# Kernel optimization log

Measured on AMD Instinct MI355X. Metric: run time of the kernel, lower is better.

The kernel has to match this reference:

```python
import jax, jax.numpy as jnp
import numpy as np

V, D, H, L, B, T = 32000, 1024, 1024, 4, 32, 128
PAD_ID = 0


def setup_inputs() -> dict:
    key = jax.random.key(0)
    ks = jax.random.split(key, 12)
    s = lambda fan: 1.0 / np.sqrt(fan)
    dec_input = jax.random.randint(ks[0], (B, T), 0, V)
    h0 = jax.random.normal(ks[1], (L, B, H), jnp.float32)
    c0 = jax.random.normal(ks[2], (L, B, H), jnp.float32)
    emb = jax.random.normal(ks[3], (V, D), jnp.float32) * 0.02
    emb = emb.at[PAD_ID].set(0.0)
    # all layers have input size H (layer0 input = embedding_dim = H)
    W_ih = jax.random.uniform(ks[4], (L, 4 * H, H), jnp.float32, -s(H), s(H))
    W_hh = jax.random.uniform(ks[5], (L, 4 * H, H), jnp.float32, -s(H), s(H))
    b_ih = jax.random.uniform(ks[6], (L, 4 * H), jnp.float32, -s(H), s(H))
    b_hh = jax.random.uniform(ks[7], (L, 4 * H), jnp.float32, -s(H), s(H))
    cls_W = jax.random.uniform(ks[8], (V, H), jnp.float32, -s(H), s(H))
    cls_b = jax.random.uniform(ks[9], (V,), jnp.float32, -s(H), s(H))
    return {"dec_input": dec_input, "h0": h0, "c0": c0, "emb": emb,
            "W_ih": W_ih, "W_hh": W_hh, "b_ih": b_ih, "b_hh": b_hh,
            "cls_W": cls_W, "cls_b": cls_b}


def _lstm_stack_step(carry, x_t, W_ih, W_hh, b_ih, b_hh):
    # carry: (h [L,B,H], c [L,B,H]); x_t: [B,H]
    h, c = carry
    inp = x_t
    hs, cs = [], []
    n_layers = W_ih.shape[0]
    for l in range(n_layers):
        gates = inp @ W_ih[l].T + h[l] @ W_hh[l].T + b_ih[l] + b_hh[l]
        i_g, f_g, g_g, o_g = jnp.split(gates, 4, axis=-1)
        c_new = jax.nn.sigmoid(f_g) * c[l] + jax.nn.sigmoid(i_g) * jnp.tanh(g_g)
        h_new = jax.nn.sigmoid(o_g) * jnp.tanh(c_new)
        inp = h_new + inp  # residual connection (dropout p=0)
        hs.append(h_new)
        cs.append(c_new)
    return (jnp.stack(hs, 0), jnp.stack(cs, 0)), inp


def reference(dec_input, h0, c0, emb, W_ih, W_hh, b_ih, b_hh, cls_W, cls_b):
    embedded = emb[dec_input]                 # [B,T,D]
    xs = jnp.swapaxes(embedded, 0, 1)         # [T,B,D]

    def step(carry, x_t):
        return _lstm_stack_step(carry, x_t, W_ih, W_hh, b_ih, b_hh)

    (hT, cT), outs = jax.lax.scan(step, (h0, c0), xs)  # outs: [T,B,H]
    outputs = jnp.swapaxes(outs, 0, 1)         # [B,T,H]
    logits = outputs @ cls_W.T + cls_b         # [B,T,V]
    return logits, (hT, cT)
```

## Files before the change

### kernel.cpp

```cpp
#include <hip/hip_runtime.h>
#include <stdint.h>

#define LAYERS 4
#define BATCH  32
#define SEQT   128
#define HID    1024
#define VOCAB  32000

typedef __attribute__((ext_vector_type(8))) short short8;
typedef __attribute__((ext_vector_type(8))) __bf16 bf16x8;
typedef __attribute__((ext_vector_type(4))) float floatx4;

#define CLS_OFF  0ul
#define X_OFF    65536000ul
#define RES_OFF  73924608ul
#define HBT_OFF  107479040ul
#define CF_OFF   141295616ul
#define SYNC_OFF 141819904ul

#define LOGITS_N 131072000ul
#define BH (BATCH * HID)

__device__ __forceinline__ unsigned short f2bf(float f) {
  union { float f; unsigned u; } v; v.f = f;
  unsigned r = v.u + 0x7FFF + ((v.u >> 16) & 1);
  return (unsigned short)(r >> 16);
}
__device__ __forceinline__ float bf2f(unsigned short b) {
  union { unsigned u; float f; } v; v.u = ((unsigned)b) << 16;
  return v.f;
}
__device__ __forceinline__ floatx4 mfma16(short8 a, short8 b, floatx4 c) {
  return __builtin_amdgcn_mfma_f32_16x16x32_bf16(
      __builtin_bit_cast(bf16x8, a), __builtin_bit_cast(bf16x8, b), c, 0, 0, 0);
}
__device__ __forceinline__ short8 cvt8(float4 a, float4 b) {
  short8 r;
  r[0] = (short)f2bf(a.x); r[1] = (short)f2bf(a.y);
  r[2] = (short)f2bf(a.z); r[3] = (short)f2bf(a.w);
  r[4] = (short)f2bf(b.x); r[5] = (short)f2bf(b.y);
  r[6] = (short)f2bf(b.z); r[7] = (short)f2bf(b.w);
  return r;
}


__global__ void k_convert(const float* __restrict__ clsw, unsigned short* __restrict__ oC) {
  const long long NC4 = 8192000LL;
  for (long long i = (long long)blockIdx.x * blockDim.x + threadIdx.x; i < NC4;
       i += (long long)gridDim.x * blockDim.x) {
    float4 v = *(const float4*)(clsw + (i << 2));
    ushort4 o; o.x = f2bf(v.x); o.y = f2bf(v.y); o.z = f2bf(v.z); o.w = f2bf(v.w);
    *(ushort4*)(oC + (i << 2)) = o;
  }
}

__global__ void k_embed(const int* __restrict__ tok, const float* __restrict__ emb,
                        unsigned short* __restrict__ X) {
  const int bt = blockIdx.x;
  const int t = bt >> 5, b = bt & 31;
  const int v = tok[b * SEQT + t];
  const float4* src = (const float4*)(emb + (size_t)v * HID);
  ushort4* dst = (ushort4*)(X + (size_t)bt * HID);
  const int i = threadIdx.x;
  float4 f = src[i];
  ushort4 o; o.x = f2bf(f.x); o.y = f2bf(f.y); o.z = f2bf(f.z); o.w = f2bf(f.w);
  dst[i] = o;
}

__global__ void k_init(const float* __restrict__ h0, const float* __restrict__ c0,
                       unsigned short* __restrict__ HBT, float* __restrict__ CF,
                       unsigned* __restrict__ sync) {
  const int i = blockIdx.x * blockDim.x + threadIdx.x;
  if (i < 4096) sync[i] = 0u;
  if (i < LAYERS * BATCH * HID) {
    HBT[i] = f2bf(h0[i]);
    CF[i] = c0[i];
  }
}


__global__ __launch_bounds__(512, 2) void k_lstm(
    const float* __restrict__ Wih, const float* __restrict__ Whh,
    const float* __restrict__ bih, const float* __restrict__ bhh,
    const unsigned short* __restrict__ X, unsigned short* __restrict__ RES,
    unsigned short* __restrict__ HBT, const float* __restrict__ CF,
    float* __restrict__ out, unsigned* __restrict__ syncp) {
  const int p = blockIdx.x;
  const int l = (p & 7) >> 1;
  const int jj = ((p >> 3) << 1) | (p & 1);
  const int j0 = jj << 4;
  const int tid = threadIdx.x;
  const int q = tid >> 6;
  const int lane = tid & 63;
  const int lo = lane & 15, hi = lane >> 4;
  const int u = tid & 15, b = tid >> 4;

  __shared__ float red[8][32][66];
  __shared__ unsigned mbx, mbh;

  if (tid == 0) { mbx = 0u; mbh = 0u; }

  (void)__hip_atomic_load(syncp + 2048, __ATOMIC_ACQUIRE, __HIP_MEMORY_SCOPE_AGENT);

  const unsigned* fx = syncp + (((l - 1) & 3) * 64 + lane) * 4;
  const unsigned* fh = syncp + (l * 64 + lane) * 4;
  unsigned* fown = syncp + (l * 64 + jj) * 4;

  short8 wx[4][4], wh[4][4];
  {
    const size_t lb = (size_t)l * 4096;
#pragma unroll
    for (int ct = 0; ct < 4; ++ct) {
#pragma unroll
      for (int ks = 0; ks < 4; ++ks) {
        const size_t off = (lb + (size_t)(ct * 1024 + j0 + lo)) * HID
                         + (size_t)q * 128 + ks * 32 + hi * 8;
        float4 a0 = *(const float4*)(Wih + off);
        float4 a1 = *(const float4*)(Wih + off + 4);
        wx[ct][ks] = cvt8(a0, a1);
        float4 b0 = *(const float4*)(Whh + off);
        float4 b1 = *(const float4*)(Whh + off + 4);
        wh[ct][ks] = cvt8(b0, b1);
      }
    }
  }
  float bias_g[4];
#pragma unroll
  for (int g = 0; g < 4; ++g)
    bias_g[g] = bih[l * 4096 + g * 1024 + j0 + u] + bhh[l * 4096 + g * 1024 + j0 + u];
  float c_reg = CF[(size_t)l * BH + (size_t)b * HID + j0 + u];

  __syncthreads();

  for (int t = 0; t < SEQT; ++t) {
    if (q == 0) {
      if (l > 0) {
        for (;;) {
          int ok = (__hip_atomic_load(fx, __ATOMIC_RELAXED, __HIP_MEMORY_SCOPE_AGENT)
                    >= (unsigned)(t + 1));
          if (__all(ok)) break;
          __builtin_amdgcn_s_sleep(1);
        }
      }
      __hip_atomic_store(&mbx, (unsigned)(t + 1),
                         __ATOMIC_RELAXED, __HIP_MEMORY_SCOPE_WORKGROUP);
    } else {
      while (__hip_atomic_load(&mbx, __ATOMIC_RELAXED, __HIP_MEMORY_SCOPE_WORKGROUP)
             < (unsigned)(t + 1))
        __builtin_amdgcn_s_sleep(1);
    }

    const unsigned short* xsrc = (l == 0)
        ? (X + (size_t)t * BH)
        : (RES + ((size_t)(l - 1) * SEQT + t) * BH);

    const unsigned short* px0 = xsrc + (size_t)lo * HID + q * 128 + hi * 8;
    const unsigned short* px1 = px0 + 16 * HID;
    const unsigned short* pxr = xsrc + (size_t)b * HID + j0 + u;

    short8 x0a, x0b, x0c, x0d, x1a, x1b, x1c, x1d;
    unsigned xres;
    asm volatile(
      "global_load_dwordx4 %0, %9,  off\n\t"
      "global_load_dwordx4 %1, %9,  off offset:64\n\t"
      "global_load_dwordx4 %2, %9,  off offset:128\n\t"
      "global_load_dwordx4 %3, %9,  off offset:192\n\t"
      "global_load_dwordx4 %4, %10, off\n\t"
      "global_load_dwordx4 %5, %10, off offset:64\n\t"
      "global_load_dwordx4 %6, %10, off offset:128\n\t"
      "global_load_dwordx4 %7, %10, off offset:192\n\t"
      "global_load_ushort  %8, %11, off\n\t"
      "s_waitcnt vmcnt(0)"
      : "=&v"(x0a), "=&v"(x0b), "=&v"(x0c), "=&v"(x0d),
        "=&v"(x1a), "=&v"(x1b), "=&v"(x1c), "=&v"(x1d), "=&v"(xres)
      : "v"(px0), "v"(px1), "v"(pxr)
      : "memory");

    floatx4 acc[4][2];
#pragma unroll
    for (int ct = 0; ct < 4; ++ct) { acc[ct][0] = {0,0,0,0}; acc[ct][1] = {0,0,0,0}; }
#pragma unroll
    for (int ct = 0; ct < 4; ++ct) {
      acc[ct][0] = mfma16(x0a, wx[ct][0], acc[ct][0]);
      acc[ct][1] = mfma16(x1a, wx[ct][0], acc[ct][1]);
      acc[ct][0] = mfma16(x0b, wx[ct][1], acc[ct][0]);
      acc[ct][1] = mfma16(x1b, wx[ct][1], acc[ct][1]);
      acc[ct][0] = mfma16(x0c, wx[ct][2], acc[ct][0]);
      acc[ct][1] = mfma16(x1c, wx[ct][2], acc[ct][1]);
      acc[ct][0] = mfma16(x0d, wx[ct][3], acc[ct][0]);
      acc[ct][1] = mfma16(x1d, wx[ct][3], acc[ct][1]);
    }

    if (q == 0) {
      if (t > 0) {
        for (;;) {
          int ok = (__hip_atomic_load(fh, __ATOMIC_RELAXED, __HIP_MEMORY_SCOPE_AGENT)
                    >= (unsigned)t);
          if (__all(ok)) break;
          __builtin_amdgcn_s_sleep(1);
        }
      }
      __hip_atomic_store(&mbh, (unsigned)(t + 1),
                         __ATOMIC_RELAXED, __HIP_MEMORY_SCOPE_WORKGROUP);
    } else {
      while (__hip_atomic_load(&mbh, __ATOMIC_RELAXED, __HIP_MEMORY_SCOPE_WORKGROUP)
             < (unsigned)(t + 1))
        __builtin_amdgcn_s_sleep(1);
    }

    const unsigned short* hsrc = HBT + ((size_t)t * LAYERS + l) * BH;
    const unsigned short* ph0 = hsrc + (size_t)lo * HID + q * 128 + hi * 8;
    const unsigned short* ph1 = ph0 + 16 * HID;

    short8 h0a, h0b, h0c, h0d, h1a, h1b, h1c, h1d;
    asm volatile(
      "global_load_dwordx4 %0, %8, off\n\t"
      "global_load_dwordx4 %1, %8, off offset:64\n\t"
      "global_load_dwordx4 %2, %8, off offset:128\n\t"
      "global_load_dwordx4 %3, %8, off offset:192\n\t"
      "global_load_dwordx4 %4, %9, off\n\t"
      "global_load_dwordx4 %5, %9, off offset:64\n\t"
      "global_load_dwordx4 %6, %9, off offset:128\n\t"
      "global_load_dwordx4 %7, %9, off offset:192\n\t"
      "s_waitcnt vmcnt(0)"
      : "=&v"(h0a), "=&v"(h0b), "=&v"(h0c), "=&v"(h0d),
        "=&v"(h1a), "=&v"(h1b), "=&v"(h1c), "=&v"(h1d)
      : "v"(ph0), "v"(ph1)
      : "memory");

#pragma unroll
    for (int ct = 0; ct < 4; ++ct) {
      acc[ct][0] = mfma16(h0a, wh[ct][0], acc[ct][0]);
      acc[ct][1] = mfma16(h1a, wh[ct][0], acc[ct][1]);
      acc[ct][0] = mfma16(h0b, wh[ct][1], acc[ct][0]);
      acc[ct][1] = mfma16(h1b, wh[ct][1], acc[ct][1]);
      acc[ct][0] = mfma16(h0c, wh[ct][2], acc[ct][0]);
      acc[ct][1] = mfma16(h1c, wh[ct][2], acc[ct][1]);
      acc[ct][0] = mfma16(h0d, wh[ct][3], acc[ct][0]);
      acc[ct][1] = mfma16(h1d, wh[ct][3], acc[ct][1]);
    }

#pragma unroll
    for (int ct = 0; ct < 4; ++ct)
#pragma unroll
      for (int rt = 0; rt < 2; ++rt)
#pragma unroll
        for (int r = 0; r < 4; ++r)
          red[q][rt * 16 + hi * 4 + r][ct * 16 + lo] = acc[ct][rt][r];
    __syncthreads();

    float gacc[4] = {0.f, 0.f, 0.f, 0.f};
#pragma unroll
    for (int qq = 0; qq < 8; ++qq)
#pragma unroll
      for (int g = 0; g < 4; ++g)
        gacc[g] += red[qq][b][g * 16 + u];

    const float ig = gacc[0] + bias_g[0];
    const float fg = gacc[1] + bias_g[1];
    const float gg = gacc[2] + bias_g[2];
    const float og = gacc[3] + bias_g[3];
    const float si = 1.f / (1.f + __expf(-ig));
    const float sf = 1.f / (1.f + __expf(-fg));
    const float so = 1.f / (1.f + __expf(-og));
    const float tg = 1.f - 2.f / (__expf(2.f * gg) + 1.f);
    const float cn = sf * c_reg + si * tg;
    const float hn = so * (1.f - 2.f / (__expf(2.f * cn) + 1.f));
    c_reg = cn;

    const float xval = bf2f((unsigned short)xres);
    const unsigned hbf = f2bf(hn);
    const unsigned rbf = f2bf(hn + xval);
    const unsigned hpk = hbf | (((unsigned)__shfl_xor((int)hbf, 1)) << 16);
    const unsigned rpk = rbf | (((unsigned)__shfl_xor((int)rbf, 1)) << 16);

    unsigned short* HBw = HBT + ((size_t)(t + 1) * LAYERS + l) * BH;
    unsigned short* RESw = RES + ((size_t)l * SEQT + t) * BH;
    const size_t hidx = (size_t)b * HID + j0 + u;
    if (!(tid & 1)) {
      __hip_atomic_store((unsigned*)(HBw + hidx), hpk,
                         __ATOMIC_RELAXED, __HIP_MEMORY_SCOPE_AGENT);
      __hip_atomic_store((unsigned*)(RESw + hidx), rpk,
                         __ATOMIC_RELAXED, __HIP_MEMORY_SCOPE_AGENT);
    }
    if (t == SEQT - 1) {
      out[LOGITS_N + (size_t)l * BH + hidx] = hn;
      out[LOGITS_N + 131072ul + (size_t)l * BH + hidx] = cn;
    }

    asm volatile("s_waitcnt vmcnt(0)" ::: "memory");
    __syncthreads();
    if (tid == 0)
      __hip_atomic_store(fown, (unsigned)(t + 1),
                         __ATOMIC_RELAXED, __HIP_MEMORY_SCOPE_AGENT);
  }
}


__global__ __launch_bounds__(256, 2) void k_cls(
    const unsigned short* __restrict__ A, const unsigned short* __restrict__ Bw,
    const float* __restrict__ bias, float* __restrict__ out) {
  __shared__ unsigned short lds_s[2][128 * 64];
  unsigned short* lA = lds_s[0];
  unsigned short* lB = lds_s[1];
  const int ntile = blockIdx.x >> 5;
  const int mtile = blockIdx.x & 31;
  const int m0 = mtile << 7, n0 = ntile << 7;
  const int tid = threadIdx.x;
  const int w = tid >> 6, lane = tid & 63, lo = lane & 15, hi = lane >> 4;
  const int mw = (w >> 1) << 6, nw = (w & 1) << 6;

  floatx4 acc[4][4];
#pragma unroll
  for (int i = 0; i < 4; ++i)
#pragma unroll
    for (int j = 0; j < 4; ++j) acc[i][j] = {0.f, 0.f, 0.f, 0.f};

  for (int k0 = 0; k0 < HID; k0 += 64) {
#pragma unroll
    for (int qq = 0; qq < 4; ++qq) {
      const int e = qq * 256 + tid;
      const int row = e >> 3, c8 = e & 7;
      const int ps = row * 64 + ((c8 ^ (row & 7)) << 3);
      *(short8*)(lA + ps) = *(const short8*)(A  + (size_t)(m0 + row) * HID + k0 + (c8 << 3));
      *(short8*)(lB + ps) = *(const short8*)(Bw + (size_t)(n0 + row) * HID + k0 + (c8 << 3));
    }
    __syncthreads();
#pragma unroll
    for (int kk = 0; kk < 2; ++kk) {
      short8 af[4], bfr[4];
#pragma unroll
      for (int x = 0; x < 4; ++x) {
        const int ra = mw + x * 16 + lo;
        af[x]  = *(const short8*)(lA + ra * 64 + ((((kk << 2) + hi) ^ (ra & 7)) << 3));
        const int rb = nw + x * 16 + lo;
        bfr[x] = *(const short8*)(lB + rb * 64 + ((((kk << 2) + hi) ^ (rb & 7)) << 3));
      }
#pragma unroll
      for (int mi = 0; mi < 4; ++mi)
#pragma unroll
        for (int ni = 0; ni < 4; ++ni)
          acc[mi][ni] = mfma16(af[mi], bfr[ni], acc[mi][ni]);
    }
    __syncthreads();
  }

  float* ldsf = (float*)lds_s;
  const int rl = tid >> 5;
  const int c4 = (tid & 31) << 2;
#pragma unroll
  for (int h = 0; h < 2; ++h) {
    __syncthreads();
    if ((mw >> 6) == h) {
#pragma unroll
      for (int mi = 0; mi < 4; ++mi)
#pragma unroll
        for (int ni = 0; ni < 4; ++ni)
#pragma unroll
          for (int r = 0; r < 4; ++r)
            ldsf[(mi * 16 + hi * 4 + r) * 128 + nw + ni * 16 + lo] = acc[mi][ni][r];
    }
    __syncthreads();
#pragma unroll
    for (int it = 0; it < 8; ++it) {
      const int lr = it * 8 + rl;
      const int ra = m0 + h * 64 + lr;
      const int orow = (ra & 31) * SEQT + (ra >> 5);
      const int v = n0 + c4;
      float4 vv = *(float4*)&ldsf[lr * 128 + c4];
      const float4 bb = *(const float4*)&bias[v];
      vv.x += bb.x; vv.y += bb.y; vv.z += bb.z; vv.w += bb.w;
      *(float4*)&out[(size_t)orow * VOCAB + v] = vv;
    }
  }
}


extern "C" void kernel_launch(void* const* d_in, const int* in_sizes, int n_in,
                              void* d_out, int out_size, void* d_ws, size_t ws_size,
                              hipStream_t stream) {
  (void)in_sizes; (void)n_in; (void)out_size; (void)ws_size;
  const int*   tok  = (const int*)d_in[0];
  const float* h0   = (const float*)d_in[1];
  const float* c0   = (const float*)d_in[2];
  const float* emb  = (const float*)d_in[3];
  const float* wih  = (const float*)d_in[4];
  const float* whh  = (const float*)d_in[5];
  const float* bih  = (const float*)d_in[6];
  const float* bhh  = (const float*)d_in[7];
  const float* clsw = (const float*)d_in[8];
  const float* clsb = (const float*)d_in[9];
  float* out = (float*)d_out;
  char* ws = (char*)d_ws;

  unsigned short* Cls = (unsigned short*)(ws + CLS_OFF);
  unsigned short* X   = (unsigned short*)(ws + X_OFF);
  unsigned short* RES = (unsigned short*)(ws + RES_OFF);
  unsigned short* HBT = (unsigned short*)(ws + HBT_OFF);
  float*          CF  = (float*)(ws + CF_OFF);
  unsigned*       SY  = (unsigned*)(ws + SYNC_OFF);

  hipLaunchKernelGGL(k_convert, dim3(2048), dim3(256), 0, stream, clsw, Cls);
  hipLaunchKernelGGL(k_embed,   dim3(SEQT * BATCH), dim3(256), 0, stream, tok, emb, X);
  hipLaunchKernelGGL(k_init,    dim3(512), dim3(256), 0, stream, h0, c0, HBT, CF, SY);

  {
    const float* a0 = wih; const float* a1 = whh; const float* a2 = bih; const float* a3 = bhh;
    const unsigned short* a4 = X; unsigned short* a5 = RES; unsigned short* a6 = HBT;
    const float* a7 = CF; float* a8 = out; unsigned* a9 = SY;
    void* kargs[] = {&a0, &a1, &a2, &a3, &a4, &a5, &a6, &a7, &a8, &a9};
    hipLaunchCooperativeKernel((void*)k_lstm, dim3(256), dim3(512), kargs, 0, stream);
  }

  hipLaunchKernelGGL(k_cls, dim3(250 * 32), dim3(256), 0, stream,
                     RES + (size_t)3 * SEQT * BATCH * HID, Cls, clsb, out);
}
```

Baseline: 1.291 ms.

## Double-buffer classifier GEMM tiles with direct global-to-LDS async loads

The classifier GEMM kernel now keeps two LDS buffers and loads the next K tile with global_load_lds while MFMAs run on the current one, replacing the synchronous global-to-register-to-LDS staging. The XOR swizzle moves from the LDS store address to the global source column, which keeps the same swizzled layout. The goal is to hide global load latency behind compute and drop the VGPR round trip. LDS use per block doubles to 64KB, which may limit occupancy under launch_bounds(256,2), and correctness depends on the manual vmcnt waits and barriers.

```diff
diff --git a/kernel.cpp b/kernel.cpp
--- a/kernel.cpp
+++ b/kernel.cpp
@@ -300,15 +300,14 @@
 __global__ __launch_bounds__(256, 2) void k_cls(
     const unsigned short* __restrict__ A, const unsigned short* __restrict__ Bw,
     const float* __restrict__ bias, float* __restrict__ out) {
-  __shared__ unsigned short lds_s[2][128 * 64];
-  unsigned short* lA = lds_s[0];
-  unsigned short* lB = lds_s[1];
+  __shared__ unsigned short lds_s[2][2][128 * 64];
   const int ntile = blockIdx.x >> 5;
   const int mtile = blockIdx.x & 31;
   const int m0 = mtile << 7, n0 = ntile << 7;
   const int tid = threadIdx.x;
   const int w = tid >> 6, lane = tid & 63, lo = lane & 15, hi = lane >> 4;
   const int mw = (w >> 1) << 6, nw = (w & 1) << 6;
+  const int wbase = w << 9;
 
   floatx4 acc[4][4];
 #pragma unroll
@@ -316,16 +315,38 @@
 #pragma unroll
     for (int j = 0; j < 4; ++j) acc[i][j] = {0.f, 0.f, 0.f, 0.f};
 
-  for (int k0 = 0; k0 < HID; k0 += 64) {
+  auto stage = [&](int buf, int k0) {
 #pragma unroll
     for (int qq = 0; qq < 4; ++qq) {
       const int e = qq * 256 + tid;
       const int row = e >> 3, c8 = e & 7;
-      const int ps = row * 64 + ((c8 ^ (row & 7)) << 3);
-      *(short8*)(lA + ps) = *(const short8*)(A  + (size_t)(m0 + row) * HID + k0 + (c8 << 3));
-      *(short8*)(lB + ps) = *(const short8*)(Bw + (size_t)(n0 + row) * HID + k0 + (c8 << 3));
-    }
-    __syncthreads();
+      const int cs = (c8 ^ (row & 7)) << 3;
+      const unsigned short* ga = A  + (size_t)(m0 + row) * HID + k0 + cs;
+      const unsigned short* gb = Bw + (size_t)(n0 + row) * HID + k0 + cs;
+      unsigned short* la = &lds_s[buf][0][0] + qq * 2048 + wbase;
+      unsigned short* lb = &lds_s[buf][1][0] + qq * 2048 + wbase;
+      __builtin_amdgcn_global_load_lds(
+          (const __attribute__((address_space(1))) unsigned*)(const void*)ga,
+          (__attribute__((address_space(3))) unsigned*)(void*)la, 16, 0, 0);
+      __builtin_amdgcn_global_load_lds(
+          (const __attribute__((address_space(1))) unsigned*)(const void*)gb,
+          (__attribute__((address_space(3))) unsigned*)(void*)lb, 16, 0, 0);
+    }
+  };
+
+  stage(0, 0);
+  for (int it = 0; it < 16; ++it) {
+    const int cur = it & 1;
+    if (it < 15) {
+      stage(cur ^ 1, (it + 1) << 6);
+      asm volatile("s_waitcnt vmcnt(8)" ::: "memory");
+    } else {
+      asm volatile("s_waitcnt vmcnt(0)" ::: "memory");
+    }
+    __builtin_amdgcn_s_barrier();
+    asm volatile("" ::: "memory");
+    const unsigned short* lA = &lds_s[cur][0][0];
+    const unsigned short* lB = &lds_s[cur][1][0];
 #pragma unroll
     for (int kk = 0; kk < 2; ++kk) {
       short8 af[4], bfr[4];
@@ -342,7 +363,8 @@
         for (int ni = 0; ni < 4; ++ni)
           acc[mi][ni] = mfma16(af[mi], bfr[ni], acc[mi][ni]);
     }
-    __syncthreads();
+    asm volatile("" ::: "memory");
+    __builtin_amdgcn_s_barrier();
   }
 
   float* ldsf = (float*)lds_s;
```

New measurement: 1.280 ms. Within noise of the previous version (-0.9%).
